# Optimization experiments

Hardware: AMD Instinct MI355X
Metric: run time of the kernel (lower is better)

The kernel has to match this reference:

```python
import jax, jax.numpy as jnp
import numpy as np

N_PTS = 100000
N_VERTS = 6890
N_JOINTS = 24


def build_rotation(q):
    # q: [N,4] unnormalized quaternions (w, x, y, z) -> [N,3,3] rotation matrices
    q = q / jnp.linalg.norm(q, axis=-1, keepdims=True)
    r, x, y, z = q[:, 0], q[:, 1], q[:, 2], q[:, 3]
    R = jnp.stack([
        1 - 2 * (y * y + z * z), 2 * (x * y - r * z), 2 * (x * z + r * y),
        2 * (x * y + r * z), 1 - 2 * (x * x + z * z), 2 * (y * z - r * x),
        2 * (x * z - r * y), 2 * (y * z + r * x), 1 - 2 * (x * x + y * y),
    ], axis=-1)
    return R.reshape(-1, 3, 3)


def setup_inputs() -> dict:
    key = jax.random.key(0)
    k1, k2, k3, k4, k5 = jax.random.split(key, 5)
    xyz = jax.random.normal(k1, (N_PTS, 3), dtype=jnp.float32)
    rotation = jax.random.normal(k2, (N_PTS, 4), dtype=jnp.float32)
    smpl_verts = jax.random.normal(k3, (N_VERTS, 3), dtype=jnp.float32)
    sw = jax.random.uniform(k4, (N_VERTS, N_JOINTS), dtype=jnp.float32)
    skinning_weights = sw / jnp.sum(sw, axis=-1, keepdims=True)  # rows sum to 1, like LBS weights
    transforms_mat = jax.random.normal(k5, (N_JOINTS, 4, 4), dtype=jnp.float32)
    return {"xyz": xyz, "rotation": rotation, "smpl_verts": smpl_verts,
            "skinning_weights": skinning_weights, "transforms_mat": transforms_mat}


def reference(xyz, rotation, smpl_verts, skinning_weights, transforms_mat):
    n_pts = xyz.shape[0]
    # --- brute-force 1-NN (knn_points, K=1) via squared Euclidean distance ---
    # d2[n, v] = |x_n|^2 - 2 x_n . v + |v|^2  -> [N, 6890]
    d2 = (jnp.sum(xyz * xyz, axis=-1, keepdims=True)
          - 2.0 * (xyz @ smpl_verts.T)
          + jnp.sum(smpl_verts * smpl_verts, axis=-1)[None, :])
    p_idx = jnp.argmin(d2, axis=-1)  # [N]
    # --- gather per-point skinning weights ---
    pts_W = skinning_weights[p_idx, :]  # [N, 24]
    # --- blend joint transforms: (N,24) @ (24,16) -> (N,4,4) ---
    T_fwd = (pts_W @ transforms_mat.reshape(-1, 16)).reshape(n_pts, 4, 4)
    # --- transform points homogeneously ---
    x_homo = jnp.concatenate([xyz, jnp.ones((n_pts, 1), dtype=xyz.dtype)], axis=-1)  # [N,4]
    x_bar = jnp.einsum('nij,nj->ni', T_fwd, x_homo)[:, :3]  # [N,3]
    # --- rotate gaussian orientations ---
    rotation_hat = build_rotation(rotation)  # [N,3,3]
    rotation_bar = jnp.einsum('nij,njk->nik', T_fwd[:, :3, :3], rotation_hat)  # [N,3,3]
    return x_bar, rotation_bar, T_fwd
```

## Files before the change

### kernel.cpp

```cpp
#include <hip/hip_runtime.h>
#include <math.h>

#define NPTS 100000
#define NVERTS 6890
#define NJ 24

#define TPB 256
#define PPT 4
#define PPB (TPB * PPT)
#define NPB ((NPTS + PPB - 1) / PPB)
#define NCH 16
#define VCH ((NVERTS + NCH - 1) / NCH)

__global__ __launch_bounds__(256, 4) void nn_kernel(
    const float* __restrict__ xyz,
    const float* __restrict__ verts,
    unsigned long long* __restrict__ best_ws)
{
#pragma clang fp contract(off)
    __shared__ float4 vlds[VCH];
    const int tid = threadIdx.x;
    const int vbase = blockIdx.y * VCH;
    const int vcnt = min(VCH, NVERTS - vbase);

    for (int i = tid; i < vcnt; i += TPB) {
        const int v = vbase + i;
        const float vx = verts[v * 3 + 0];
        const float vy = verts[v * 3 + 1];
        const float vz = verts[v * 3 + 2];
        vlds[i] = make_float4(vx, vy, vz, (vx * vx + vy * vy) + vz * vz);
    }
    __syncthreads();

    const int p0 = blockIdx.x * PPB + tid;
    float px[PPT], py[PPT], pz[PPT], xsq[PPT], best[PPT];
    int bidx[PPT];
    #pragma unroll
    for (int k = 0; k < PPT; ++k) {
        const int p = p0 + k * TPB;
        const int pc = (p < NPTS) ? p : (NPTS - 1);
        px[k] = xyz[pc * 3 + 0];
        py[k] = xyz[pc * 3 + 1];
        pz[k] = xyz[pc * 3 + 2];
        xsq[k] = (px[k] * px[k] + py[k] * py[k]) + pz[k] * pz[k];
        best[k] = 1e30f;
        bidx[k] = 0;
    }

    #pragma unroll 2
    for (int i = 0; i < vcnt; ++i) {
        const float4 v = vlds[i];
        #pragma unroll
        for (int k = 0; k < PPT; ++k) {
            float g = px[k] * v.x;
            g = fmaf(py[k], v.y, g);
            g = fmaf(pz[k], v.z, g);
            const float t = fmaf(-2.0f, g, xsq[k]);
            const float d2 = t + v.w;
            const bool lt = (d2 < best[k]);
            best[k] = lt ? d2 : best[k];
            bidx[k] = lt ? (vbase + i) : bidx[k];
        }
    }

    #pragma unroll
    for (int k = 0; k < PPT; ++k) {
        const int p = p0 + k * TPB;
        if (p < NPTS) {
            const unsigned long long pk =
                ((unsigned long long)__float_as_uint(best[k]) << 32) |
                (unsigned int)bidx[k];
            atomicMin(&best_ws[p], pk);
        }
    }
}

__global__ __launch_bounds__(256) void apply_kernel(
    const float* __restrict__ xyz,
    const float* __restrict__ rot,
    const float* __restrict__ sw,
    const float* __restrict__ tm,
    const unsigned long long* __restrict__ best_ws,
    float* __restrict__ out)
{
    __shared__ float tl[NJ * 16];
    const int tid = threadIdx.x;
    for (int i = tid; i < NJ * 16; i += 256) tl[i] = tm[i];
    __syncthreads();

    const int p = blockIdx.x * 256 + tid;
    if (p >= NPTS) return;

    const int vi = (int)(best_ws[p] & 0xFFFFFFFFull);
    const float4* w4 = reinterpret_cast<const float4*>(sw + (size_t)vi * NJ);

    float T[16];
    #pragma unroll
    for (int i = 0; i < 16; ++i) T[i] = 0.0f;

    #pragma unroll
    for (int jq = 0; jq < NJ / 4; ++jq) {
        const float4 wv = w4[jq];
        const float wj[4] = { wv.x, wv.y, wv.z, wv.w };
        #pragma unroll
        for (int k = 0; k < 4; ++k) {
            const int j = jq * 4 + k;
            #pragma unroll
            for (int i = 0; i < 16; ++i)
                T[i] = fmaf(wj[k], tl[j * 16 + i], T[i]);
        }
    }

    const float4 q = reinterpret_cast<const float4*>(rot)[p];
    float qr = q.x, qx = q.y, qy = q.z, qz = q.w;
    const float inv = 1.0f / sqrtf(qr * qr + qx * qx + qy * qy + qz * qz);
    qr *= inv; qx *= inv; qy *= inv; qz *= inv;
    float R[9];
    R[0] = 1.0f - 2.0f * (qy * qy + qz * qz);
    R[1] = 2.0f * (qx * qy - qr * qz);
    R[2] = 2.0f * (qx * qz + qr * qy);
    R[3] = 2.0f * (qx * qy + qr * qz);
    R[4] = 1.0f - 2.0f * (qx * qx + qz * qz);
    R[5] = 2.0f * (qy * qz - qr * qx);
    R[6] = 2.0f * (qx * qz - qr * qy);
    R[7] = 2.0f * (qy * qz + qr * qx);
    R[8] = 1.0f - 2.0f * (qx * qx + qy * qy);

    const float x0 = xyz[p * 3 + 0];
    const float x1 = xyz[p * 3 + 1];
    const float x2 = xyz[p * 3 + 2];

    #pragma unroll
    for (int i = 0; i < 3; ++i) {
        out[p * 3 + i] = fmaf(T[i * 4 + 0], x0,
                          fmaf(T[i * 4 + 1], x1,
                           fmaf(T[i * 4 + 2], x2, T[i * 4 + 3])));
    }

    float* rb = out + 300000 + (size_t)p * 9;
    #pragma unroll
    for (int i = 0; i < 3; ++i) {
        #pragma unroll
        for (int k = 0; k < 3; ++k) {
            rb[i * 3 + k] = fmaf(T[i * 4 + 0], R[0 * 3 + k],
                             fmaf(T[i * 4 + 1], R[1 * 3 + k],
                                  T[i * 4 + 2] * R[2 * 3 + k]));
        }
    }

    float* tb = out + 1200000 + (size_t)p * 16;
    #pragma unroll
    for (int i = 0; i < 16; ++i) tb[i] = T[i];
}

extern "C" void kernel_launch(void* const* d_in, const int* in_sizes, int n_in,
                              void* d_out, int out_size, void* d_ws, size_t ws_size,
                              hipStream_t stream) {
    const float* xyz   = (const float*)d_in[0];
    const float* rot   = (const float*)d_in[1];
    const float* verts = (const float*)d_in[2];
    const float* sw    = (const float*)d_in[3];
    const float* tm    = (const float*)d_in[4];
    float* out = (float*)d_out;

    unsigned long long* best_ws = (unsigned long long*)d_ws;

    hipMemsetAsync(d_ws, 0xFF, NPTS * sizeof(unsigned long long), stream);

    dim3 grid(NPB, NCH);
    nn_kernel<<<grid, TPB, 0, stream>>>(xyz, verts, best_ws);
    apply_kernel<<<(NPTS + 255) / 256, 256, 0, stream>>>(xyz, rot, sw, tm, best_ws, out);
}
```

Baseline: 145.1 us.

## Split NN search into 21 padded vertex chunks with prefetched LDS loads

Splits the vertex set into 21 chunks of stride 329. Each chunk scans a fixed 336 entries, and the padding entries carry w=1e30 so they never win. Occupancy is raised to 6 blocks per SIMD via launch bounds. The inner loop is hand-unrolled with scalarised per-point registers, fminf updates and double-buffered float4 LDS reads. The aim is to hide LDS latency, drop bounds checks and raise parallelism, at the cost of a few redundant overlapping vertices per chunk and more atomics.

New measurement: 182.9 us. 1.26x slower.

```diff
diff --git a/kernel.cpp b/kernel.cpp
--- a/kernel.cpp
+++ b/kernel.cpp
@@ -9,70 +9,84 @@
 #define PPT 4
 #define PPB (TPB * PPT)
 #define NPB ((NPTS + PPB - 1) / PPB)
-#define NCH 16
-#define VCH ((NVERTS + NCH - 1) / NCH)
+#define NCH 21
+#define STRIDE 329
+#define ITER 336
+#define LDSN 344
 
-__global__ __launch_bounds__(256, 4) void nn_kernel(
+__global__ __launch_bounds__(256, 6) void nn_kernel(
     const float* __restrict__ xyz,
     const float* __restrict__ verts,
     unsigned long long* __restrict__ best_ws)
 {
 #pragma clang fp contract(off)
-    __shared__ float4 vlds[VCH];
+    __shared__ float4 vlds[LDSN];
     const int tid = threadIdx.x;
-    const int vbase = blockIdx.y * VCH;
-    const int vcnt = min(VCH, NVERTS - vbase);
+    const int vbase = blockIdx.y * STRIDE;
 
-    for (int i = tid; i < vcnt; i += TPB) {
+    for (int i = tid; i < LDSN; i += TPB) {
         const int v = vbase + i;
-        const float vx = verts[v * 3 + 0];
-        const float vy = verts[v * 3 + 1];
-        const float vz = verts[v * 3 + 2];
-        vlds[i] = make_float4(vx, vy, vz, (vx * vx + vy * vy) + vz * vz);
+        if (v < NVERTS) {
+            const float vx = verts[v * 3 + 0];
+            const float vy = verts[v * 3 + 1];
+            const float vz = verts[v * 3 + 2];
+            vlds[i] = make_float4(vx, vy, vz, (vx * vx + vy * vy) + vz * vz);
+        } else {
+            vlds[i] = make_float4(0.0f, 0.0f, 0.0f, 1e30f);
+        }
     }
     __syncthreads();
 
     const int p0 = blockIdx.x * PPB + tid;
-    float px[PPT], py[PPT], pz[PPT], xsq[PPT], best[PPT];
-    int bidx[PPT];
-    #pragma unroll
-    for (int k = 0; k < PPT; ++k) {
-        const int p = p0 + k * TPB;
-        const int pc = (p < NPTS) ? p : (NPTS - 1);
-        px[k] = xyz[pc * 3 + 0];
-        py[k] = xyz[pc * 3 + 1];
-        pz[k] = xyz[pc * 3 + 2];
-        xsq[k] = (px[k] * px[k] + py[k] * py[k]) + pz[k] * pz[k];
-        best[k] = 1e30f;
-        bidx[k] = 0;
+    float px0, py0, pz0, xs0, px1, py1, pz1, xs1;
+    float px2, py2, pz2, xs2, px3, py3, pz3, xs3;
+    float bs0 = 1e30f, bs1 = 1e30f, bs2 = 1e30f, bs3 = 1e30f;
+    int bi0 = 0, bi1 = 0, bi2 = 0, bi3 = 0;
+
+#define LOADPT(K) { \
+    const int p = p0 + (K) * TPB; \
+    const int pc = (p < NPTS) ? p : (NPTS - 1); \
+    px##K = xyz[pc * 3 + 0]; py##K = xyz[pc * 3 + 1]; pz##K = xyz[pc * 3 + 2]; \
+    xs##K = (px##K * px##K + py##K * py##K) + pz##K * pz##K; }
+    LOADPT(0) LOADPT(1) LOADPT(2) LOADPT(3)
+#undef LOADPT
+
+#define STEP(V, VI) { \
+    const int vi_ = (VI); \
+    { float g = px0 * (V).x; g = fmaf(py0, (V).y, g); g = fmaf(pz0, (V).z, g); \
+      const float d = fmaf(-2.0f, g, xs0) + (V).w; \
+      bi0 = (d < bs0) ? vi_ : bi0; bs0 = fminf(bs0, d); } \
+    { float g = px1 * (V).x; g = fmaf(py1, (V).y, g); g = fmaf(pz1, (V).z, g); \
+      const float d = fmaf(-2.0f, g, xs1) + (V).w; \
+      bi1 = (d < bs1) ? vi_ : bi1; bs1 = fminf(bs1, d); } \
+    { float g = px2 * (V).x; g = fmaf(py2, (V).y, g); g = fmaf(pz2, (V).z, g); \
+      const float d = fmaf(-2.0f, g, xs2) + (V).w; \
+      bi2 = (d < bs2) ? vi_ : bi2; bs2 = fminf(bs2, d); } \
+    { float g = px3 * (V).x; g = fmaf(py3, (V).y, g); g = fmaf(pz3, (V).z, g); \
+      const float d = fmaf(-2.0f, g, xs3) + (V).w; \
+      bi3 = (d < bs3) ? vi_ : bi3; bs3 = fminf(bs3, d); } }
+
+    float4 a0 = vlds[0], a1 = vlds[1], a2 = vlds[2], a3 = vlds[3];
+    #pragma unroll 1
+    for (int i = 0; i + 8 <= ITER; i += 8) {
+        float4 b0 = vlds[i + 4], b1 = vlds[i + 5], b2 = vlds[i + 6], b3 = vlds[i + 7];
+        STEP(a0, vbase + i + 0) STEP(a1, vbase + i + 1)
+        STEP(a2, vbase + i + 2) STEP(a3, vbase + i + 3)
+        a0 = vlds[i + 8]; a1 = vlds[i + 9]; a2 = vlds[i + 10]; a3 = vlds[i + 11];
+        STEP(b0, vbase + i + 4) STEP(b1, vbase + i + 5)
+        STEP(b2, vbase + i + 6) STEP(b3, vbase + i + 7)
     }
+#undef STEP
 
-    #pragma unroll 2
-    for (int i = 0; i < vcnt; ++i) {
-        const float4 v = vlds[i];
-        #pragma unroll
-        for (int k = 0; k < PPT; ++k) {
-            float g = px[k] * v.x;
-            g = fmaf(py[k], v.y, g);
-            g = fmaf(pz[k], v.z, g);
-            const float t = fmaf(-2.0f, g, xsq[k]);
-            const float d2 = t + v.w;
-            const bool lt = (d2 < best[k]);
-            best[k] = lt ? d2 : best[k];
-            bidx[k] = lt ? (vbase + i) : bidx[k];
-        }
-    }
-
-    #pragma unroll
-    for (int k = 0; k < PPT; ++k) {
-        const int p = p0 + k * TPB;
-        if (p < NPTS) {
-            const unsigned long long pk =
-                ((unsigned long long)__float_as_uint(best[k]) << 32) |
-                (unsigned int)bidx[k];
-            atomicMin(&best_ws[p], pk);
-        }
-    }
+#define FLUSH(K) { \
+    const int p = p0 + (K) * TPB; \
+    if (p < NPTS) { \
+        const unsigned long long pk = \
+            ((unsigned long long)__float_as_uint(bs##K) << 32) | (unsigned int)bi##K; \
+        atomicMin(&best_ws[p], pk); \
+    } }
+    FLUSH(0) FLUSH(1) FLUSH(2) FLUSH(3)
+#undef FLUSH
 }
 
 __global__ __launch_bounds__(256) void apply_kernel(
```

## Compute nearest-neighbor distances with split-bf16 MFMA and exact fp32 refinement

Applied to the files above, without the earlier changes.

Replaces the scalar FP32 brute-force nearest-neighbor search with a two-pass scheme on matrix cores. Vertices and points are each split into bf16 high/low parts, and 32x32x16 bf16 MFMAs compute approximate distances. A first pass finds each point's approximate minimum. A second pass recomputes those distances and, for every candidate under a tolerance threshold, does an exact fp32 distance and an atomicMin. This trades the fp32 ALU-bound inner loop for matrix-core throughput, at the cost of an extra prep kernel, two full passes, atomics, and risk of tie or precision mismatches against the reference.

New measurement: 161.1 us. 11.0% more time.

```diff
diff --git a/kernel.cpp b/kernel.cpp
--- a/kernel.cpp
+++ b/kernel.cpp
@@ -5,72 +5,142 @@
 #define NVERTS 6890
 #define NJ 24
 
-#define TPB 256
-#define PPT 4
-#define PPB (TPB * PPT)
-#define NPB ((NPTS + PPB - 1) / PPB)
-#define NCH 16
-#define VCH ((NVERTS + NCH - 1) / NCH)
-
-__global__ __launch_bounds__(256, 4) void nn_kernel(
+#define NTILE 216
+#define CPT 24
+#define NCHK 9
+#define TILE_F4 96
+#define CHUNK_F4 (CPT * TILE_F4)
+#define REC_F4 (NCHK * CHUNK_F4)
+
+typedef short bf16x8 __attribute__((ext_vector_type(8)));
+typedef float f32x16 __attribute__((ext_vector_type(16)));
+
+__device__ __forceinline__ unsigned short bf16_rtne(float f) {
+    const unsigned int u = __float_as_uint(f);
+    return (unsigned short)((u + 0x7FFFu + ((u >> 16) & 1u)) >> 16);
+}
+__device__ __forceinline__ float bf16_back(unsigned short h) {
+    return __uint_as_float(((unsigned int)h) << 16);
+}
+__device__ __forceinline__ float min16(const f32x16 a) {
+    float t0 = fminf(a[0], a[1]),  t1 = fminf(a[2], a[3]);
+    float t2 = fminf(a[4], a[5]),  t3 = fminf(a[6], a[7]);
+    float t4 = fminf(a[8], a[9]),  t5 = fminf(a[10], a[11]);
+    float t6 = fminf(a[12], a[13]), t7 = fminf(a[14], a[15]);
+    t0 = fminf(t0, t1); t2 = fminf(t2, t3); t4 = fminf(t4, t5); t6 = fminf(t6, t7);
+    return fminf(fminf(t0, t2), fminf(t4, t6));
+}
+
+__global__ void prep_kernel(const float* __restrict__ verts, float4* __restrict__ recG)
+{
+#pragma clang fp contract(off)
+    const int v = blockIdx.x * 256 + threadIdx.x;
+    if (v >= NTILE * 32) return;
+    const int t_glob = v >> 5, row = v & 31;
+    float4* base = recG + (t_glob / CPT) * CHUNK_F4 + (t_glob % CPT) * TILE_F4;
+
+    float cx = 0.f, cy = 0.f, cz = 0.f, vsq;
+    unsigned short vh0, vh1, vh2, vl0, vl1, vl2, qh, ql;
+    const short one = (short)0x3F80;
+    if (v < NVERTS) {
+        cx = verts[v * 3 + 0]; cy = verts[v * 3 + 1]; cz = verts[v * 3 + 2];
+        vsq = (cx * cx + cy * cy) + cz * cz;
+        vh0 = bf16_rtne(cx); vl0 = bf16_rtne(cx - bf16_back(vh0));
+        vh1 = bf16_rtne(cy); vl1 = bf16_rtne(cy - bf16_back(vh1));
+        vh2 = bf16_rtne(cz); vl2 = bf16_rtne(cz - bf16_back(vh2));
+        qh = bf16_rtne(vsq); ql = bf16_rtne(vsq - bf16_back(qh));
+    } else {
+        vh0 = vh1 = vh2 = vl0 = vl1 = vl2 = 0;
+        qh = bf16_rtne(30000.0f); ql = 0; vsq = 1e30f;
+    }
+    union { bf16x8 s; float4 f; } r0, r1;
+    r0.s = (bf16x8){(short)vh0, (short)vh1, (short)vh2,
+                    (short)vl0, (short)vl1, (short)vl2, (short)vh0, (short)vh1};
+    r1.s = (bf16x8){(short)vh2, (short)qh, (short)ql, one, one, 0, 0, 0};
+    base[row]      = r0.f;
+    base[32 + row] = r1.f;
+    base[64 + row] = make_float4(cx, cy, cz, vsq);
+}
+
+__global__ __launch_bounds__(256) void nn_mfma_kernel(
     const float* __restrict__ xyz,
-    const float* __restrict__ verts,
+    const float4* __restrict__ recG,
     unsigned long long* __restrict__ best_ws)
 {
 #pragma clang fp contract(off)
-    __shared__ float4 vlds[VCH];
+    __shared__ float4 smem[CHUNK_F4];
     const int tid = threadIdx.x;
-    const int vbase = blockIdx.y * VCH;
-    const int vcnt = min(VCH, NVERTS - vbase);
-
-    for (int i = tid; i < vcnt; i += TPB) {
-        const int v = vbase + i;
-        const float vx = verts[v * 3 + 0];
-        const float vy = verts[v * 3 + 1];
-        const float vz = verts[v * 3 + 2];
-        vlds[i] = make_float4(vx, vy, vz, (vx * vx + vy * vy) + vz * vz);
-    }
-    __syncthreads();
-
-    const int p0 = blockIdx.x * PPB + tid;
-    float px[PPT], py[PPT], pz[PPT], xsq[PPT], best[PPT];
-    int bidx[PPT];
-    #pragma unroll
-    for (int k = 0; k < PPT; ++k) {
-        const int p = p0 + k * TPB;
-        const int pc = (p < NPTS) ? p : (NPTS - 1);
-        px[k] = xyz[pc * 3 + 0];
-        py[k] = xyz[pc * 3 + 1];
-        pz[k] = xyz[pc * 3 + 2];
-        xsq[k] = (px[k] * px[k] + py[k] * py[k]) + pz[k] * pz[k];
-        best[k] = 1e30f;
-        bidx[k] = 0;
-    }
-
-    #pragma unroll 2
-    for (int i = 0; i < vcnt; ++i) {
-        const float4 v = vlds[i];
-        #pragma unroll
-        for (int k = 0; k < PPT; ++k) {
-            float g = px[k] * v.x;
-            g = fmaf(py[k], v.y, g);
-            g = fmaf(pz[k], v.z, g);
-            const float t = fmaf(-2.0f, g, xsq[k]);
-            const float d2 = t + v.w;
-            const bool lt = (d2 < best[k]);
-            best[k] = lt ? d2 : best[k];
-            bidx[k] = lt ? (vbase + i) : bidx[k];
-        }
-    }
-
-    #pragma unroll
-    for (int k = 0; k < PPT; ++k) {
-        const int p = p0 + k * TPB;
-        if (p < NPTS) {
-            const unsigned long long pk =
-                ((unsigned long long)__float_as_uint(best[k]) << 32) |
-                (unsigned int)bidx[k];
-            atomicMin(&best_ws[p], pk);
+    const int lane = tid & 63;
+    const int wid = tid >> 6;
+    const int half = lane >> 5;
+    const int col = lane & 31;
+
+    const int p = blockIdx.x * 128 + wid * 32 + col;
+    const int pe = (p < NPTS) ? p : (NPTS - 1);
+    const float x = xyz[pe * 3 + 0], y = xyz[pe * 3 + 1], z = xyz[pe * 3 + 2];
+    const float xsq = (x * x + y * y) + z * z;
+
+    const float ux = -2.0f * x, uy = -2.0f * y, uz = -2.0f * z;
+    const unsigned short uh0 = bf16_rtne(ux), uh1 = bf16_rtne(uy), uh2 = bf16_rtne(uz);
+    const unsigned short ul0 = bf16_rtne(ux - bf16_back(uh0));
+    const unsigned short ul1 = bf16_rtne(uy - bf16_back(uh1));
+    const unsigned short ul2 = bf16_rtne(uz - bf16_back(uh2));
+    const unsigned short qh = bf16_rtne(xsq);
+    const unsigned short ql = bf16_rtne(xsq - bf16_back(qh));
+    const short one = (short)0x3F80;
+    bf16x8 bfrag;
+    if (half == 0)
+        bfrag = (bf16x8){(short)uh0, (short)uh1, (short)uh2,
+                         (short)uh0, (short)uh1, (short)uh2, (short)ul0, (short)ul1};
+    else
+        bfrag = (bf16x8){(short)ul2, one, one, (short)qh, (short)ql, 0, 0, 0};
+
+    const f32x16 zacc = {0.f};
+    const int aidx = half * 32 + col;
+
+    float run = 1e30f;
+    for (int c = 0; c < NCHK; ++c) {
+        __syncthreads();
+        const float4* src = recG + c * CHUNK_F4;
+        for (int i = tid; i < CHUNK_F4; i += 256) smem[i] = src[i];
+        __syncthreads();
+        for (int t = 0; t < CPT; ++t) {
+            union { float4 f; bf16x8 s; } a;
+            a.f = smem[t * TILE_F4 + aidx];
+            const f32x16 acc = __builtin_amdgcn_mfma_f32_32x32x16_bf16(a.s, bfrag, zacc, 0, 0, 0);
+            run = fminf(run, min16(acc));
+        }
+    }
+    const float m = fminf(run, __shfl_xor(run, 32));
+    const float thr = m + (1.5e-4f + 1.5e-4f * xsq + 1.0e-4f * m);
+
+    for (int c = 0; c < NCHK; ++c) {
+        __syncthreads();
+        const float4* src = recG + c * CHUNK_F4;
+        for (int i = tid; i < CHUNK_F4; i += 256) smem[i] = src[i];
+        __syncthreads();
+        for (int t = 0; t < CPT; ++t) {
+            union { float4 f; bf16x8 s; } a;
+            a.f = smem[t * TILE_F4 + aidx];
+            const f32x16 acc = __builtin_amdgcn_mfma_f32_32x32x16_bf16(a.s, bfrag, zacc, 0, 0, 0);
+            if (min16(acc) <= thr) {
+                #pragma unroll
+                for (int e = 0; e < 16; ++e) {
+                    if (acc[e] <= thr) {
+                        const int row = (e & 3) + 8 * (e >> 2) + 4 * half;
+                        const float4 vr = smem[t * TILE_F4 + 64 + row];
+                        float g = x * vr.x;
+                        g = fmaf(y, vr.y, g);
+                        g = fmaf(z, vr.z, g);
+                        const float tt = fmaf(-2.0f, g, xsq);
+                        const float d2 = tt + vr.w;
+                        const int vg = c * (CPT * 32) + t * 32 + row;
+                        const unsigned long long pk =
+                            ((unsigned long long)__float_as_uint(d2) << 32) | (unsigned)vg;
+                        atomicMin(&best_ws[pe], pk);
+                    }
+                }
+            }
         }
     }
 }
@@ -164,10 +234,11 @@
     float* out = (float*)d_out;
 
     unsigned long long* best_ws = (unsigned long long*)d_ws;
+    float4* recG = (float4*)((char*)d_ws + (1 << 20));
 
     hipMemsetAsync(d_ws, 0xFF, NPTS * sizeof(unsigned long long), stream);
 
-    dim3 grid(NPB, NCH);
-    nn_kernel<<<grid, TPB, 0, stream>>>(xyz, verts, best_ws);
+    prep_kernel<<<(NTILE * 32 + 255) / 256, 256, 0, stream>>>(verts, recG);
+    nn_mfma_kernel<<<(NPTS + 127) / 128, 256, 0, stream>>>(xyz, recG, best_ws);
     apply_kernel<<<(NPTS + 255) / 256, 256, 0, stream>>>(xyz, rot, sw, tm, best_ws, out);
 }
```
